# Kernel tuning notes

Hardware: AMD Instinct MI355X
Metric: run time of the kernel (lower is better)

The kernel has to match this reference:

```python
import jax, jax.numpy as jnp
import numpy as np

D_MODEL = 1024
HEAD_DIM = D_MODEL // 16  # num_heads=16, used only for the softmax scale
EPS = 1e-5


def _layernorm(x, g, b):
    mu = jnp.mean(x, axis=-1, keepdims=True)
    var = jnp.var(x, axis=-1, keepdims=True)
    return (x - mu) * jax.lax.rsqrt(var + EPS) * g + b


def setup_inputs() -> dict:
    key = jax.random.key(0)
    ks = jax.random.split(key, 16)
    d, dff = D_MODEL, 4 * D_MODEL
    s = 1.0 / np.sqrt(d)
    inp = {
        "x": jax.random.normal(ks[0], (4, 2048, d), dtype=jnp.float32),
        "wq": jax.random.normal(ks[1], (d, d), dtype=jnp.float32) * s,
        "bq": jnp.zeros((d,), jnp.float32),
        "wk": jax.random.normal(ks[2], (d, d), dtype=jnp.float32) * s,
        "bk": jnp.zeros((d,), jnp.float32),
        "wv": jax.random.normal(ks[3], (d, d), dtype=jnp.float32) * s,
        "bv": jnp.zeros((d,), jnp.float32),
        "wo": jax.random.normal(ks[4], (d, d), dtype=jnp.float32) * s,
        "bo": jnp.zeros((d,), jnp.float32),
        "w1": jax.random.normal(ks[5], (d, dff), dtype=jnp.float32) * s,
        "b1": jnp.zeros((dff,), jnp.float32),
        "w2": jax.random.normal(ks[6], (dff, d), dtype=jnp.float32) * (1.0 / np.sqrt(dff)),
        "b2": jnp.zeros((d,), jnp.float32),
        "g1": jnp.ones((d,), jnp.float32),
        "be1": jnp.zeros((d,), jnp.float32),
        "g2": jnp.ones((d,), jnp.float32),
        "be2": jnp.zeros((d,), jnp.float32),
    }
    return inp


def reference(x, wq, bq, wk, bk, wv, bv, wo, bo, w1, b1, w2, b2, g1, be1, g2, be2):
    # --- attention sub-block (NOTE: no head split in original module) ---
    residual = x
    h = _layernorm(x, g1, be1)
    q = h @ wq + bq
    k = h @ wk + bk
    v = h @ wv + bv
    scale = 1.0 / np.sqrt(HEAD_DIM)
    scores = jnp.einsum("bsd,btd->bst", q, k) * scale  # [B,S,S]
    attn = jax.nn.softmax(scores, axis=-1)
    ctx = jnp.einsum("bst,btd->bsd", attn, v)
    x = ctx @ wo + bo + residual
    # --- MLP sub-block ---
    residual = x
    h = _layernorm(x, g2, be2)
    h = jax.nn.gelu(h @ w1 + b1, approximate=False)
    return h @ w2 + b2 + residual
```

## Files before the change

### kernel.cpp

```cpp
#include <hip/hip_runtime.h>
#include <hip/hip_bf16.h>

typedef __hip_bfloat16 bf16;
typedef __attribute__((ext_vector_type(8))) short short8;
typedef __attribute__((ext_vector_type(4))) float floatx4;

__device__ __forceinline__ unsigned short f2bf(float x) {
  unsigned u = __builtin_bit_cast(unsigned, x);
  unsigned r = (u + 0x7fffu + ((u >> 16) & 1u)) >> 16;
  return (unsigned short)r;
}

#define GLL(g, l) __builtin_amdgcn_global_load_lds(                                  \
    (const __attribute__((address_space(1))) void*)(g),                              \
    (__attribute__((address_space(3))) void*)(l), 16, 0, 0)

__global__ __launch_bounds__(256) void wtrans_kernel(const float* __restrict__ in,
                                                     bf16* __restrict__ out,
                                                     int K, int N) {
  __shared__ float tile[32][33];
  int tx = threadIdx.x, ty = threadIdx.y;
  int n0 = blockIdx.x * 32, k0 = blockIdx.y * 32;
#pragma unroll
  for (int i = 0; i < 32; i += 8)
    tile[ty + i][tx] = in[(size_t)(k0 + ty + i) * N + (n0 + tx)];
  __syncthreads();
#pragma unroll
  for (int i = 0; i < 32; i += 8)
    out[(size_t)(n0 + ty + i) * K + (k0 + tx)] = __float2bfloat16(tile[tx][ty + i]);
}

__global__ __launch_bounds__(256) void btrans_kernel(const bf16* __restrict__ in,
                                                     int ldin, size_t sIn,
                                                     bf16* __restrict__ out,
                                                     int ldout, size_t sOut) {
  __shared__ bf16 tile[32][33];
  int tx = threadIdx.x, ty = threadIdx.y;
  int c0 = blockIdx.x * 32, r0 = blockIdx.y * 32;
  size_t bi = sIn * blockIdx.z, bo = sOut * blockIdx.z;
#pragma unroll
  for (int i = 0; i < 32; i += 8)
    tile[ty + i][tx] = in[bi + (size_t)(r0 + ty + i) * ldin + (c0 + tx)];
  __syncthreads();
#pragma unroll
  for (int i = 0; i < 32; i += 8)
    out[bo + (size_t)(c0 + ty + i) * ldout + (r0 + tx)] = tile[tx][ty + i];
}

__global__ __launch_bounds__(256) void ln_kernel(const float* __restrict__ x,
                                                 const float* __restrict__ g,
                                                 const float* __restrict__ b,
                                                 bf16* __restrict__ out) {
  const int D = 1024;
  size_t row = blockIdx.x;
  int t = threadIdx.x;
  float4 v = ((const float4*)(x + row * D))[t];
  float s  = v.x + v.y + v.z + v.w;
  float ss = v.x * v.x + v.y * v.y + v.z * v.z + v.w * v.w;
#pragma unroll
  for (int off = 32; off > 0; off >>= 1) {
    s  += __shfl_xor(s, off);
    ss += __shfl_xor(ss, off);
  }
  __shared__ float rs[4], rss[4];
  int wv = t >> 6;
  if ((t & 63) == 0) { rs[wv] = s; rss[wv] = ss; }
  __syncthreads();
  s  = rs[0] + rs[1] + rs[2] + rs[3];
  ss = rss[0] + rss[1] + rss[2] + rss[3];
  float mu  = s * (1.f / D);
  float inv = rsqrtf(ss * (1.f / D) - mu * mu + 1e-5f);
  float4 gv = ((const float4*)g)[t];
  float4 bv = ((const float4*)b)[t];
  ushort4 o;
  o.x = f2bf((v.x - mu) * inv * gv.x + bv.x);
  o.y = f2bf((v.y - mu) * inv * gv.y + bv.y);
  o.z = f2bf((v.z - mu) * inv * gv.z + bv.z);
  o.w = f2bf((v.w - mu) * inv * gv.w + bv.w);
  ((ushort4*)(out + row * D))[t] = o;
}

__global__ __launch_bounds__(256) void softmax_kernel(float* sc) {
  const int S = 2048;
  float* p = sc + (size_t)blockIdx.x * S;
  int t = threadIdx.x;
  float4 v0 = ((const float4*)p)[2 * t];
  float4 v1 = ((const float4*)p)[2 * t + 1];
  float f[8] = {v0.x, v0.y, v0.z, v0.w, v1.x, v1.y, v1.z, v1.w};
  float m = f[0];
#pragma unroll
  for (int j = 1; j < 8; ++j) m = fmaxf(m, f[j]);
#pragma unroll
  for (int off = 32; off > 0; off >>= 1) m = fmaxf(m, __shfl_xor(m, off));
  __shared__ float r1[4], r2[4];
  int wv = t >> 6;
  if ((t & 63) == 0) r1[wv] = m;
  __syncthreads();
  m = fmaxf(fmaxf(r1[0], r1[1]), fmaxf(r1[2], r1[3]));
  float s = 0.f;
#pragma unroll
  for (int j = 0; j < 8; ++j) { f[j] = __expf(f[j] - m); s += f[j]; }
#pragma unroll
  for (int off = 32; off > 0; off >>= 1) s += __shfl_xor(s, off);
  if ((t & 63) == 0) r2[wv] = s;
  __syncthreads();
  s = r2[0] + r2[1] + r2[2] + r2[3];
  float inv = 1.f / s;
  unsigned u0 = f2bf(f[0] * inv), u1 = f2bf(f[1] * inv);
  unsigned u2 = f2bf(f[2] * inv), u3 = f2bf(f[3] * inv);
  unsigned u4 = f2bf(f[4] * inv), u5 = f2bf(f[5] * inv);
  unsigned u6 = f2bf(f[6] * inv), u7 = f2bf(f[7] * inv);
  uint4 o;
  o.x = u0 | (u1 << 16);
  o.y = u2 | (u3 << 16);
  o.z = u4 | (u5 << 16);
  o.w = u6 | (u7 << 16);
  ((uint4*)p)[t] = o;
}

template <int NF, bool OUT_BF16, bool HAS_BIAS, bool HAS_RES, bool GELU>
__global__ __launch_bounds__(512, 2) void gemm8p(
    const bf16* __restrict__ A, int lda, size_t sA,
    const bf16* __restrict__ BT, int ldb, size_t sB,
    void* Cv, size_t sC,
    const float* __restrict__ bias, const float* res,
    int N, int K, float alpha, int gx, int gy) {
  constexpr int BN = NF * 64;
  constexpr int LB = NF / 2;
  constexpr int VM = 4 + 3 * LB;
  constexpr int BSLOT = BN * 64;
  __shared__ char lds[65536 + 4 * BSLOT + 1024];
  char* const ldsA = lds;
  char* const ldsB = lds + 65536;
  char* const ldsScr = lds + 65536 + 4 * BSLOT;

  const int tid = threadIdx.x;
  const int lane = tid & 63;
  const int wave = tid >> 6;
  const int wm = wave >> 2, wn = wave & 3;
  const int lr = lane & 15, lq = lane >> 4;

  int id = blockIdx.x;
  const int nwg = gridDim.x;
  if ((nwg & 7) == 0) id = (id & 7) * (nwg >> 3) + (id >> 3);
  const int bx = id % gx;
  const int rem = id / gx;
  const int by = rem % gy;
  const int bz = rem / gy;
  const int m0 = by * 256, n0 = bx * BN;

  const int wrow = wave * 16 + (lane >> 2);
  const int swzc = ((lane & 3) ^ ((lane >> 2) & 3)) * 8;
  const bf16* gA = A + sA * bz + (size_t)(m0 + wrow) * lda + swzc;
  const bf16* gB = BT + sB * bz + (size_t)(n0 + wrow) * ldb + swzc;

  const int nk = K >> 6;

  const int aBase = (wm * 128 + lr) * 64 + ((lq ^ (lr & 3)) << 4);
  const int bBase = (wn * (NF * 16) + lr) * 64 + ((lq ^ (lr & 3)) << 4);

  auto stA = [&](int tau, int h) {
    const int tc = tau < nk ? tau : nk - 1;
    const bf16* s = gA + (size_t)tc * 64 + h * 32;
    if (tau < nk) {
      char* d = ldsA + (((tau & 1) * 2 + h) << 14) + tid * 16;
      GLL(s, d);
      GLL(s + (size_t)128 * lda, d + 8192);
    } else {
      char* d = ldsScr + (lane << 4);
      GLL(s, d);
      GLL(s, d);
    }
  };
  auto stB = [&](int tau, int h) {
    const int tc = tau < nk ? tau : nk - 1;
    const bf16* s = gB + (size_t)tc * 64 + h * 32;
    if (tau < nk) {
      char* d = ldsB + ((tau & 1) * 2 + h) * BSLOT + tid * 16;
      GLL(s, d);
      if constexpr (NF == 4) GLL(s + (size_t)128 * ldb, d + 8192);
    } else {
      char* d = ldsScr + (lane << 4);
      GLL(s, d);
      if constexpr (NF == 4) GLL(s, d);
    }
  };

  floatx4 acc[8][NF] = {};

  stB(0, 0); stA(0, 0); stB(0, 1); stA(0, 1);
  stB(1, 0); stA(1, 0); stB(1, 1);
  asm volatile("s_waitcnt vmcnt(%0)" ::"i"(VM) : "memory");
  __builtin_amdgcn_s_barrier();

  for (int t = 0; t < nk; ++t) {
    const char* Ak0 = ldsA + (((t & 1) * 2 + 0) << 14);
    const char* Ak1 = ldsA + (((t & 1) * 2 + 1) << 14);
    const char* Bk0 = ldsB + ((t & 1) * 2 + 0) * BSLOT;
    const char* Bk1 = ldsB + ((t & 1) * 2 + 1) * BSLOT;

    short8 b0[NF], a0[4];
#pragma unroll
    for (int ni = 0; ni < NF; ++ni) b0[ni] = *(const short8*)(Bk0 + bBase + ni * 1024);
#pragma unroll
    for (int mi = 0; mi < 4; ++mi) a0[mi] = *(const short8*)(Ak0 + aBase + mi * 1024);
    stA(t + 1, 1);
    __builtin_amdgcn_s_barrier();
    asm volatile("s_waitcnt lgkmcnt(0)" ::: "memory");
    __builtin_amdgcn_sched_barrier(0);
    __builtin_amdgcn_s_setprio(1);
#pragma unroll
    for (int mi = 0; mi < 4; ++mi)
#pragma unroll
      for (int ni = 0; ni < NF; ++ni)
        acc[mi][ni] = __builtin_amdgcn_mfma_f32_16x16x32_bf16(a0[mi], b0[ni], acc[mi][ni], 0, 0, 0);
    __builtin_amdgcn_s_setprio(0);
    __builtin_amdgcn_s_barrier();

    short8 a1[4];
#pragma unroll
    for (int mi = 0; mi < 4; ++mi) a1[mi] = *(const short8*)(Ak0 + aBase + 4096 + mi * 1024);
    stB(t + 2, 0);
    __builtin_amdgcn_s_barrier();
    asm volatile("s_waitcnt lgkmcnt(0)" ::: "memory");
    __builtin_amdgcn_sched_barrier(0);
    __builtin_amdgcn_s_setprio(1);
#pragma unroll
    for (int mi = 0; mi < 4; ++mi)
#pragma unroll
      for (int ni = 0; ni < NF; ++ni)
        acc[4 + mi][ni] = __builtin_amdgcn_mfma_f32_16x16x32_bf16(a1[mi], b0[ni], acc[4 + mi][ni], 0, 0, 0);
    __builtin_amdgcn_s_setprio(0);
    asm volatile("s_waitcnt vmcnt(%0)" ::"i"(VM) : "memory");
    __builtin_amdgcn_s_barrier();

    short8 b1[NF], a2[4];
#pragma unroll
    for (int ni = 0; ni < NF; ++ni) b1[ni] = *(const short8*)(Bk1 + bBase + ni * 1024);
#pragma unroll
    for (int mi = 0; mi < 4; ++mi) a2[mi] = *(const short8*)(Ak1 + aBase + mi * 1024);
    stA(t + 2, 0);
    __builtin_amdgcn_s_barrier();
    asm volatile("s_waitcnt lgkmcnt(0)" ::: "memory");
    __builtin_amdgcn_sched_barrier(0);
    __builtin_amdgcn_s_setprio(1);
#pragma unroll
    for (int mi = 0; mi < 4; ++mi)
#pragma unroll
      for (int ni = 0; ni < NF; ++ni)
        acc[mi][ni] = __builtin_amdgcn_mfma_f32_16x16x32_bf16(a2[mi], b1[ni], acc[mi][ni], 0, 0, 0);
    __builtin_amdgcn_s_setprio(0);
    __builtin_amdgcn_s_barrier();

    short8 a3[4];
#pragma unroll
    for (int mi = 0; mi < 4; ++mi) a3[mi] = *(const short8*)(Ak1 + aBase + 4096 + mi * 1024);
    stB(t + 2, 1);
    __builtin_amdgcn_s_barrier();
    asm volatile("s_waitcnt lgkmcnt(0)" ::: "memory");
    __builtin_amdgcn_sched_barrier(0);
    __builtin_amdgcn_s_setprio(1);
#pragma unroll
    for (int mi = 0; mi < 4; ++mi)
#pragma unroll
      for (int ni = 0; ni < NF; ++ni)
        acc[4 + mi][ni] = __builtin_amdgcn_mfma_f32_16x16x32_bf16(a3[mi], b1[ni], acc[4 + mi][ni], 0, 0, 0);
    __builtin_amdgcn_s_setprio(0);
    asm volatile("s_waitcnt vmcnt(%0)" ::"i"(VM) : "memory");
    __builtin_amdgcn_s_barrier();
  }
  asm volatile("s_waitcnt vmcnt(0)" ::: "memory");

  float* Cf = (float*)Cv;
  bf16* Cb = (bf16*)Cv;
  const size_t cb = sC * bz;
#pragma unroll
  for (int mi = 0; mi < 8; ++mi) {
    const int row = m0 + wm * 128 + mi * 16 + lq * 4;
#pragma unroll
    for (int ni = 0; ni < NF; ++ni) {
      const int col = n0 + wn * (NF * 16) + ni * 16 + lr;
      const float bb = HAS_BIAS ? bias[col] : 0.f;
#pragma unroll
      for (int r = 0; r < 4; ++r) {
        float val = acc[mi][ni][r] * alpha + bb;
        if (GELU) val = 0.5f * val * (1.f + erff(val * 0.70710678118654752f));
        if (HAS_RES) val += res[(size_t)(row + r) * N + col];
        const size_t idx = cb + (size_t)(row + r) * N + col;
        if (OUT_BF16) Cb[idx] = __float2bfloat16(val);
        else Cf[idx] = val;
      }
    }
  }
}

extern "C" void kernel_launch(void* const* d_in, const int* in_sizes, int n_in,
                              void* d_out, int out_size, void* d_ws, size_t ws_size,
                              hipStream_t stream) {
  const int B = 4, S = 2048, D = 1024, DFF = 4096;
  const int M = B * S;
  const float* x   = (const float*)d_in[0];
  const float* wq  = (const float*)d_in[1];
  const float* bq  = (const float*)d_in[2];
  const float* wk  = (const float*)d_in[3];
  const float* bk  = (const float*)d_in[4];
  const float* wv  = (const float*)d_in[5];
  const float* bv  = (const float*)d_in[6];
  const float* wo  = (const float*)d_in[7];
  const float* bo  = (const float*)d_in[8];
  const float* w1  = (const float*)d_in[9];
  const float* b1  = (const float*)d_in[10];
  const float* w2  = (const float*)d_in[11];
  const float* b2  = (const float*)d_in[12];
  const float* g1  = (const float*)d_in[13];
  const float* be1 = (const float*)d_in[14];
  const float* g2  = (const float*)d_in[15];
  const float* be2 = (const float*)d_in[16];
  float* out = (float*)d_out;

  char* wsb = (char*)d_ws;
  const size_t MB1 = 1ull << 20;
  bf16* wqkvT = (bf16*)(wsb + 0 * MB1);
  bf16* woT   = (bf16*)(wsb + 6 * MB1);
  bf16* w1T   = (bf16*)(wsb + 8 * MB1);
  bf16* w2T   = (bf16*)(wsb + 16 * MB1);
  float* bqkv = (float*)(wsb + 24 * MB1);
  bf16* h     = (bf16*)(wsb + 25 * MB1);
  bf16* qkv   = (bf16*)(wsb + 41 * MB1);
  bf16* hidden = (bf16*)(wsb + 41 * MB1);
  char* attn  = wsb + 89 * MB1;

  int chunk = 1;
  if (ws_size > 89 * MB1) {
    size_t c = (ws_size - 89 * MB1) / (20 * MB1);
    chunk = (int)(c > 4 ? 4 : (c < 1 ? 1 : c));
  }
  bf16* vTc = (bf16*)attn;
  float* sc = (float*)(attn + (size_t)chunk * 4 * MB1);

  dim3 tb(32, 8);
  wtrans_kernel<<<dim3(32, 32), tb, 0, stream>>>(wq, wqkvT, D, D);
  wtrans_kernel<<<dim3(32, 32), tb, 0, stream>>>(wk, wqkvT + (size_t)1024 * 1024, D, D);
  wtrans_kernel<<<dim3(32, 32), tb, 0, stream>>>(wv, wqkvT + (size_t)2048 * 1024, D, D);
  wtrans_kernel<<<dim3(32, 32), tb, 0, stream>>>(wo, woT, D, D);
  wtrans_kernel<<<dim3(128, 32), tb, 0, stream>>>(w1, w1T, D, DFF);
  wtrans_kernel<<<dim3(32, 128), tb, 0, stream>>>(w2, w2T, DFF, D);
  hipMemcpyAsync(bqkv, bq, 4096, hipMemcpyDeviceToDevice, stream);
  hipMemcpyAsync(bqkv + 1024, bk, 4096, hipMemcpyDeviceToDevice, stream);
  hipMemcpyAsync(bqkv + 2048, bv, 4096, hipMemcpyDeviceToDevice, stream);

  ln_kernel<<<M, 256, 0, stream>>>(x, g1, be1, h);

  gemm8p<2, true, true, false, false><<<24 * 32, 512, 0, stream>>>(
      h, D, 0, wqkvT, D, 0, qkv, 0, bqkv, nullptr, 3072, D, 1.f, 24, 32);

  for (int b0 = 0; b0 < B; b0 += chunk) {
    int c = (B - b0 < chunk) ? (B - b0) : chunk;
    btrans_kernel<<<dim3(32, 64, c), tb, 0, stream>>>(
        qkv + (size_t)b0 * S * 3072 + 2048, 3072, (size_t)S * 3072,
        vTc, S, (size_t)D * S);
    gemm8p<4, false, false, false, false><<<64 * c, 512, 0, stream>>>(
        qkv + (size_t)b0 * S * 3072, 3072, (size_t)S * 3072,
        qkv + (size_t)b0 * S * 3072 + 1024, 3072, (size_t)S * 3072,
        sc, (size_t)S * S, nullptr, nullptr, S, D, 0.125f, 8, 8);
    softmax_kernel<<<c * S, 256, 0, stream>>>(sc);
    gemm8p<2, true, false, false, false><<<64 * c, 512, 0, stream>>>(
        (const bf16*)sc, 2 * S, (size_t)S * 2 * S,
        vTc, S, (size_t)D * S,
        h + (size_t)b0 * S * D, (size_t)S * D, nullptr, nullptr, D, S, 1.f, 8, 8);
  }

  gemm8p<2, false, true, true, false><<<8 * 32, 512, 0, stream>>>(
      h, D, 0, woT, D, 0, out, 0, bo, x, D, D, 1.f, 8, 32);

  ln_kernel<<<M, 256, 0, stream>>>(out, g2, be2, h);

  gemm8p<4, true, true, false, true><<<16 * 32, 512, 0, stream>>>(
      h, D, 0, w1T, D, 0, hidden, 0, b1, nullptr, DFF, D, 1.f, 16, 32);

  gemm8p<2, false, true, true, false><<<8 * 32, 512, 0, stream>>>(
      hidden, DFF, 0, w2T, DFF, 0, out, 0, b2, out, D, DFF, 1.f, 8, 32);
}
```

Before: 492.0 us.

## Restructure GEMM into quadrant-pipelined tiles and fuse V transpose into QKV epilogue

```diff
diff --git a/kernel.cpp b/kernel.cpp
--- a/kernel.cpp
+++ b/kernel.cpp
@@ -14,6 +14,10 @@
 #define GLL(g, l) __builtin_amdgcn_global_load_lds(                                  \
     (const __attribute__((address_space(1))) void*)(g),                              \
     (__attribute__((address_space(3))) void*)(l), 16, 0, 0)
+
+template <int N> __device__ __forceinline__ void vmwait() {
+  asm volatile("s_waitcnt vmcnt(%0)" ::"i"(N) : "memory");
+}
 
 __global__ __launch_bounds__(256) void wtrans_kernel(const float* __restrict__ in,
                                                      bf16* __restrict__ out,
@@ -28,23 +32,6 @@
 #pragma unroll
   for (int i = 0; i < 32; i += 8)
     out[(size_t)(n0 + ty + i) * K + (k0 + tx)] = __float2bfloat16(tile[tx][ty + i]);
-}
-
-__global__ __launch_bounds__(256) void btrans_kernel(const bf16* __restrict__ in,
-                                                     int ldin, size_t sIn,
-                                                     bf16* __restrict__ out,
-                                                     int ldout, size_t sOut) {
-  __shared__ bf16 tile[32][33];
-  int tx = threadIdx.x, ty = threadIdx.y;
-  int c0 = blockIdx.x * 32, r0 = blockIdx.y * 32;
-  size_t bi = sIn * blockIdx.z, bo = sOut * blockIdx.z;
-#pragma unroll
-  for (int i = 0; i < 32; i += 8)
-    tile[ty + i][tx] = in[bi + (size_t)(r0 + ty + i) * ldin + (c0 + tx)];
-  __syncthreads();
-#pragma unroll
-  for (int i = 0; i < 32; i += 8)
-    out[bo + (size_t)(c0 + ty + i) * ldout + (r0 + tx)] = tile[tx][ty + i];
 }
 
 __global__ __launch_bounds__(256) void ln_kernel(const float* __restrict__ x,
@@ -118,21 +105,21 @@
   ((uint4*)p)[t] = o;
 }
 
-template <int NF, bool OUT_BF16, bool HAS_BIAS, bool HAS_RES, bool GELU>
-__global__ __launch_bounds__(512, 2) void gemm8p(
+template <int NF, bool OUT_BF16, bool HAS_BIAS, bool HAS_RES, bool GELU, bool VTR>
+__global__ __launch_bounds__(512, 2) void gemm4q(
     const bf16* __restrict__ A, int lda, size_t sA,
     const bf16* __restrict__ BT, int ldb, size_t sB,
     void* Cv, size_t sC,
-    const float* __restrict__ bias, const float* res,
+    const float* __restrict__ bias, const float* res, bf16* vtr,
     int N, int K, float alpha, int gx, int gy) {
   constexpr int BN = NF * 64;
-  constexpr int LB = NF / 2;
-  constexpr int VM = 4 + 3 * LB;
-  constexpr int BSLOT = BN * 64;
-  __shared__ char lds[65536 + 4 * BSLOT + 1024];
+  constexpr int NI = NF / 2;
+  constexpr int BHALF = NF == 4 ? 16384 : 8192;
+  constexpr int W_A = 4;
+  constexpr int W_B = NF == 4 ? 4 : 3;
+  __shared__ __align__(16) char lds[65536 + (NF == 4 ? 65536 : 32768)];
   char* const ldsA = lds;
   char* const ldsB = lds + 65536;
-  char* const ldsScr = lds + 65536 + 4 * BSLOT;
 
   const int tid = threadIdx.x;
   const int lane = tid & 63;
@@ -149,149 +136,178 @@
   const int bz = rem / gy;
   const int m0 = by * 256, n0 = bx * BN;
 
-  const int wrow = wave * 16 + (lane >> 2);
-  const int swzc = ((lane & 3) ^ ((lane >> 2) & 3)) * 8;
-  const bf16* gA = A + sA * bz + (size_t)(m0 + wrow) * lda + swzc;
-  const bf16* gB = BT + sB * bz + (size_t)(n0 + wrow) * ldb + swzc;
+  const int srow = tid >> 3;
+  const int schunk = ((tid & 7) ^ (srow & 7)) * 8;
+  const bf16* gA = A + sA * bz + (size_t)(m0 + srow) * lda + schunk;
+  const bf16* gB = BT + sB * bz + (size_t)(n0 + srow) * ldb + schunk;
 
   const int nk = K >> 6;
 
-  const int aBase = (wm * 128 + lr) * 64 + ((lq ^ (lr & 3)) << 4);
-  const int bBase = (wn * (NF * 16) + lr) * 64 + ((lq ^ (lr & 3)) << 4);
-
-  auto stA = [&](int tau, int h) {
-    const int tc = tau < nk ? tau : nk - 1;
-    const bf16* s = gA + (size_t)tc * 64 + h * 32;
-    if (tau < nk) {
-      char* d = ldsA + (((tau & 1) * 2 + h) << 14) + tid * 16;
+  auto stA = [&](int tt, int h) {
+    if (tt < nk) {
+      const bf16* s = gA + (size_t)(h * 128) * lda + (size_t)tt * 64;
+      char* d = ldsA + (((tt & 1) * 2 + h) << 14) + tid * 16;
       GLL(s, d);
-      GLL(s + (size_t)128 * lda, d + 8192);
-    } else {
-      char* d = ldsScr + (lane << 4);
+      GLL(s + (size_t)64 * lda, d + 8192);
+    }
+  };
+  auto stB = [&](int tt, int h) {
+    if (tt < nk) {
+      const bf16* s = gB + (size_t)(h * (BN / 2)) * ldb + (size_t)tt * 64;
+      char* d = ldsB + ((tt & 1) * 2 + h) * BHALF + tid * 16;
       GLL(s, d);
-      GLL(s, d);
+      if constexpr (NF == 4) GLL(s + (size_t)64 * ldb, d + 8192);
     }
   };
-  auto stB = [&](int tau, int h) {
-    const int tc = tau < nk ? tau : nk - 1;
-    const bf16* s = gB + (size_t)tc * 64 + h * 32;
-    if (tau < nk) {
-      char* d = ldsB + ((tau & 1) * 2 + h) * BSLOT + tid * 16;
-      GLL(s, d);
-      if constexpr (NF == 4) GLL(s + (size_t)128 * ldb, d + 8192);
-    } else {
-      char* d = ldsScr + (lane << 4);
-      GLL(s, d);
-      if constexpr (NF == 4) GLL(s, d);
-    }
-  };
-
-  floatx4 acc[8][NF] = {};
-
-  stB(0, 0); stA(0, 0); stB(0, 1); stA(0, 1);
-  stB(1, 0); stA(1, 0); stB(1, 1);
-  asm volatile("s_waitcnt vmcnt(%0)" ::"i"(VM) : "memory");
+
+  const int aB0 = (wm * 64 + lr) * 128 + ((lq ^ (lr & 7)) << 4);
+  const int aB1 = aB0 ^ 64;
+  const int bRow = (NF == 4) ? (wn * 32 + lr) : (wn * 16 + lr);
+  const int bB0 = bRow * 128 + ((lq ^ (lr & 7)) << 4);
+  const int bB1 = bB0 ^ 64;
+
+  floatx4 acc[2][2][4][NI] = {};
+
+  stA(0, 0); stB(0, 0); stB(0, 1); stA(0, 1);
+  vmwait<W_B>();
   __builtin_amdgcn_s_barrier();
 
   for (int t = 0; t < nk; ++t) {
-    const char* Ak0 = ldsA + (((t & 1) * 2 + 0) << 14);
-    const char* Ak1 = ldsA + (((t & 1) * 2 + 1) << 14);
-    const char* Bk0 = ldsB + ((t & 1) * 2 + 0) * BSLOT;
-    const char* Bk1 = ldsB + ((t & 1) * 2 + 1) * BSLOT;
-
-    short8 b0[NF], a0[4];
-#pragma unroll
-    for (int ni = 0; ni < NF; ++ni) b0[ni] = *(const short8*)(Bk0 + bBase + ni * 1024);
-#pragma unroll
-    for (int mi = 0; mi < 4; ++mi) a0[mi] = *(const short8*)(Ak0 + aBase + mi * 1024);
-    stA(t + 1, 1);
-    __builtin_amdgcn_s_barrier();
+    const char* As0 = ldsA + (((t & 1) * 2 + 0) << 14);
+    const char* As1 = ldsA + (((t & 1) * 2 + 1) << 14);
+    const char* Bs0 = ldsB + ((t & 1) * 2 + 0) * BHALF;
+    const char* Bs1 = ldsB + ((t & 1) * 2 + 1) * BHALF;
+    short8 a0[4], a1[4], b0[NI], b1[NI];
+
+#pragma unroll
+    for (int mi = 0; mi < 4; ++mi) {
+      a0[mi] = *(const short8*)(As0 + aB0 + mi * 2048);
+      a1[mi] = *(const short8*)(As0 + aB1 + mi * 2048);
+    }
+#pragma unroll
+    for (int ni = 0; ni < NI; ++ni) {
+      b0[ni] = *(const short8*)(Bs0 + bB0 + ni * 2048);
+      b1[ni] = *(const short8*)(Bs0 + bB1 + ni * 2048);
+    }
+    stA(t + 1, 0);
     asm volatile("s_waitcnt lgkmcnt(0)" ::: "memory");
     __builtin_amdgcn_sched_barrier(0);
     __builtin_amdgcn_s_setprio(1);
 #pragma unroll
     for (int mi = 0; mi < 4; ++mi)
 #pragma unroll
-      for (int ni = 0; ni < NF; ++ni)
-        acc[mi][ni] = __builtin_amdgcn_mfma_f32_16x16x32_bf16(a0[mi], b0[ni], acc[mi][ni], 0, 0, 0);
+      for (int ni = 0; ni < NI; ++ni)
+        acc[0][0][mi][ni] = __builtin_amdgcn_mfma_f32_16x16x32_bf16(a0[mi], b0[ni], acc[0][0][mi][ni], 0, 0, 0);
+#pragma unroll
+    for (int mi = 0; mi < 4; ++mi)
+#pragma unroll
+      for (int ni = 0; ni < NI; ++ni)
+        acc[0][0][mi][ni] = __builtin_amdgcn_mfma_f32_16x16x32_bf16(a1[mi], b1[ni], acc[0][0][mi][ni], 0, 0, 0);
     __builtin_amdgcn_s_setprio(0);
+    vmwait<W_A>();
     __builtin_amdgcn_s_barrier();
 
-    short8 a1[4];
-#pragma unroll
-    for (int mi = 0; mi < 4; ++mi) a1[mi] = *(const short8*)(Ak0 + aBase + 4096 + mi * 1024);
-    stB(t + 2, 0);
-    __builtin_amdgcn_s_barrier();
+#pragma unroll
+    for (int ni = 0; ni < NI; ++ni) {
+      b0[ni] = *(const short8*)(Bs1 + bB0 + ni * 2048);
+      b1[ni] = *(const short8*)(Bs1 + bB1 + ni * 2048);
+    }
+    stB(t + 1, 0);
     asm volatile("s_waitcnt lgkmcnt(0)" ::: "memory");
     __builtin_amdgcn_sched_barrier(0);
     __builtin_amdgcn_s_setprio(1);
 #pragma unroll
     for (int mi = 0; mi < 4; ++mi)
 #pragma unroll
-      for (int ni = 0; ni < NF; ++ni)
-        acc[4 + mi][ni] = __builtin_amdgcn_mfma_f32_16x16x32_bf16(a1[mi], b0[ni], acc[4 + mi][ni], 0, 0, 0);
+      for (int ni = 0; ni < NI; ++ni)
+        acc[0][1][mi][ni] = __builtin_amdgcn_mfma_f32_16x16x32_bf16(a0[mi], b0[ni], acc[0][1][mi][ni], 0, 0, 0);
+#pragma unroll
+    for (int mi = 0; mi < 4; ++mi)
+#pragma unroll
+      for (int ni = 0; ni < NI; ++ni)
+        acc[0][1][mi][ni] = __builtin_amdgcn_mfma_f32_16x16x32_bf16(a1[mi], b1[ni], acc[0][1][mi][ni], 0, 0, 0);
     __builtin_amdgcn_s_setprio(0);
-    asm volatile("s_waitcnt vmcnt(%0)" ::"i"(VM) : "memory");
+    vmwait<W_B>();
     __builtin_amdgcn_s_barrier();
 
-    short8 b1[NF], a2[4];
-#pragma unroll
-    for (int ni = 0; ni < NF; ++ni) b1[ni] = *(const short8*)(Bk1 + bBase + ni * 1024);
-#pragma unroll
-    for (int mi = 0; mi < 4; ++mi) a2[mi] = *(const short8*)(Ak1 + aBase + mi * 1024);
-    stA(t + 2, 0);
-    __builtin_amdgcn_s_barrier();
+#pragma unroll
+    for (int mi = 0; mi < 4; ++mi) {
+      a0[mi] = *(const short8*)(As1 + aB0 + mi * 2048);
+      a1[mi] = *(const short8*)(As1 + aB1 + mi * 2048);
+    }
+    stB(t + 1, 1);
     asm volatile("s_waitcnt lgkmcnt(0)" ::: "memory");
     __builtin_amdgcn_sched_barrier(0);
     __builtin_amdgcn_s_setprio(1);
 #pragma unroll
     for (int mi = 0; mi < 4; ++mi)
 #pragma unroll
-      for (int ni = 0; ni < NF; ++ni)
-        acc[mi][ni] = __builtin_amdgcn_mfma_f32_16x16x32_bf16(a2[mi], b1[ni], acc[mi][ni], 0, 0, 0);
+      for (int ni = 0; ni < NI; ++ni)
+        acc[1][1][mi][ni] = __builtin_amdgcn_mfma_f32_16x16x32_bf16(a0[mi], b0[ni], acc[1][1][mi][ni], 0, 0, 0);
+#pragma unroll
+    for (int mi = 0; mi < 4; ++mi)
+#pragma unroll
+      for (int ni = 0; ni < NI; ++ni)
+        acc[1][1][mi][ni] = __builtin_amdgcn_mfma_f32_16x16x32_bf16(a1[mi], b1[ni], acc[1][1][mi][ni], 0, 0, 0);
     __builtin_amdgcn_s_setprio(0);
     __builtin_amdgcn_s_barrier();
 
-    short8 a3[4];
-#pragma unroll
-    for (int mi = 0; mi < 4; ++mi) a3[mi] = *(const short8*)(Ak1 + aBase + 4096 + mi * 1024);
-    stB(t + 2, 1);
-    __builtin_amdgcn_s_barrier();
+#pragma unroll
+    for (int ni = 0; ni < NI; ++ni) {
+      b0[ni] = *(const short8*)(Bs0 + bB0 + ni * 2048);
+      b1[ni] = *(const short8*)(Bs0 + bB1 + ni * 2048);
+    }
+    stA(t + 1, 1);
     asm volatile("s_waitcnt lgkmcnt(0)" ::: "memory");
     __builtin_amdgcn_sched_barrier(0);
     __builtin_amdgcn_s_setprio(1);
 #pragma unroll
     for (int mi = 0; mi < 4; ++mi)
 #pragma unroll
-      for (int ni = 0; ni < NF; ++ni)
-        acc[4 + mi][ni] = __builtin_amdgcn_mfma_f32_16x16x32_bf16(a3[mi], b1[ni], acc[4 + mi][ni], 0, 0, 0);
+      for (int ni = 0; ni < NI; ++ni)
+        acc[1][0][mi][ni] = __builtin_amdgcn_mfma_f32_16x16x32_bf16(a0[mi], b0[ni], acc[1][0][mi][ni], 0, 0, 0);
+#pragma unroll
+    for (int mi = 0; mi < 4; ++mi)
+#pragma unroll
+      for (int ni = 0; ni < NI; ++ni)
+        acc[1][0][mi][ni] = __builtin_amdgcn_mfma_f32_16x16x32_bf16(a1[mi], b1[ni], acc[1][0][mi][ni], 0, 0, 0);
     __builtin_amdgcn_s_setprio(0);
-    asm volatile("s_waitcnt vmcnt(%0)" ::"i"(VM) : "memory");
+    vmwait<W_B>();
     __builtin_amdgcn_s_barrier();
   }
-  asm volatile("s_waitcnt vmcnt(0)" ::: "memory");
 
   float* Cf = (float*)Cv;
   bf16* Cb = (bf16*)Cv;
   const size_t cb = sC * bz;
 #pragma unroll
-  for (int mi = 0; mi < 8; ++mi) {
-    const int row = m0 + wm * 128 + mi * 16 + lq * 4;
-#pragma unroll
-    for (int ni = 0; ni < NF; ++ni) {
-      const int col = n0 + wn * (NF * 16) + ni * 16 + lr;
-      const float bb = HAS_BIAS ? bias[col] : 0.f;
-#pragma unroll
-      for (int r = 0; r < 4; ++r) {
-        float val = acc[mi][ni][r] * alpha + bb;
-        if (GELU) val = 0.5f * val * (1.f + erff(val * 0.70710678118654752f));
-        if (HAS_RES) val += res[(size_t)(row + r) * N + col];
-        const size_t idx = cb + (size_t)(row + r) * N + col;
-        if (OUT_BF16) Cb[idx] = __float2bfloat16(val);
-        else Cf[idx] = val;
+  for (int mq = 0; mq < 2; ++mq)
+#pragma unroll
+    for (int nq = 0; nq < 2; ++nq)
+#pragma unroll
+      for (int mi = 0; mi < 4; ++mi) {
+        const int row = m0 + mq * 128 + wm * 64 + mi * 16 + lq * 4;
+#pragma unroll
+        for (int ni = 0; ni < NI; ++ni) {
+          const int col = n0 + nq * (BN / 2) + wn * (BN / 8) + ni * 16 + lr;
+          const float bb = HAS_BIAS ? bias[col] : 0.f;
+#pragma unroll
+          for (int r = 0; r < 4; ++r) {
+            float val = acc[mq][nq][mi][ni][r] * alpha + bb;
+            if (GELU) val = 0.5f * val * (1.f + erff(val * 0.70710678118654752f));
+            if (HAS_RES) val += res[(size_t)(row + r) * N + col];
+            const size_t idx = cb + (size_t)(row + r) * N + col;
+            if (OUT_BF16) Cb[idx] = __float2bfloat16(val);
+            else Cf[idx] = val;
+            if (VTR) {
+              if (col >= 2048) {
+                const int rr = row + r;
+                vtr[(((size_t)(rr >> 11) << 10) + (col - 2048)) * 2048 + (rr & 2047)] =
+                    __float2bfloat16(val);
+              }
+            }
+          }
+        }
       }
-    }
-  }
 }
 
 extern "C" void kernel_launch(void* const* d_in, const int* in_sizes, int n_in,
@@ -328,15 +344,14 @@
   bf16* h     = (bf16*)(wsb + 25 * MB1);
   bf16* qkv   = (bf16*)(wsb + 41 * MB1);
   bf16* hidden = (bf16*)(wsb + 41 * MB1);
-  char* attn  = wsb + 89 * MB1;
+  bf16* vTall = (bf16*)(wsb + 89 * MB1);
+  float* sc   = (float*)(wsb + 105 * MB1);
 
   int chunk = 1;
-  if (ws_size > 89 * MB1) {
-    size_t c = (ws_size - 89 * MB1) / (20 * MB1);
+  if (ws_size > 105 * MB1) {
+    size_t c = (ws_size - 105 * MB1) / (16 * MB1);
     chunk = (int)(c > 4 ? 4 : (c < 1 ? 1 : c));
   }
-  bf16* vTc = (bf16*)attn;
-  float* sc = (float*)(attn + (size_t)chunk * 4 * MB1);
 
   dim3 tb(32, 8);
   wtrans_kernel<<<dim3(32, 32), tb, 0, stream>>>(wq, wqkvT, D, D);
@@ -351,33 +366,30 @@
 
   ln_kernel<<<M, 256, 0, stream>>>(x, g1, be1, h);
 
-  gemm8p<2, true, true, false, false><<<24 * 32, 512, 0, stream>>>(
-      h, D, 0, wqkvT, D, 0, qkv, 0, bqkv, nullptr, 3072, D, 1.f, 24, 32);
+  gemm4q<2, true, true, false, false, true><<<24 * 32, 512, 0, stream>>>(
+      h, D, 0, wqkvT, D, 0, qkv, 0, bqkv, nullptr, vTall, 3072, D, 1.f, 24, 32);
 
   for (int b0 = 0; b0 < B; b0 += chunk) {
     int c = (B - b0 < chunk) ? (B - b0) : chunk;
-    btrans_kernel<<<dim3(32, 64, c), tb, 0, stream>>>(
-        qkv + (size_t)b0 * S * 3072 + 2048, 3072, (size_t)S * 3072,
-        vTc, S, (size_t)D * S);
-    gemm8p<4, false, false, false, false><<<64 * c, 512, 0, stream>>>(
+    gemm4q<4, false, false, false, false, false><<<64 * c, 512, 0, stream>>>(
         qkv + (size_t)b0 * S * 3072, 3072, (size_t)S * 3072,
         qkv + (size_t)b0 * S * 3072 + 1024, 3072, (size_t)S * 3072,
-        sc, (size_t)S * S, nullptr, nullptr, S, D, 0.125f, 8, 8);
+        sc, (size_t)S * S, nullptr, nullptr, nullptr, S, D, 0.125f, 8, 8);
     softmax_kernel<<<c * S, 256, 0, stream>>>(sc);
-    gemm8p<2, true, false, false, false><<<64 * c, 512, 0, stream>>>(
+    gemm4q<2, true, false, false, false, false><<<64 * c, 512, 0, stream>>>(
         (const bf16*)sc, 2 * S, (size_t)S * 2 * S,
-        vTc, S, (size_t)D * S,
-        h + (size_t)b0 * S * D, (size_t)S * D, nullptr, nullptr, D, S, 1.f, 8, 8);
+        vTall + (size_t)b0 * D * S, S, (size_t)D * S,
+        h + (size_t)b0 * S * D, (size_t)S * D, nullptr, nullptr, nullptr, D, S, 1.f, 8, 8);
   }
 
-  gemm8p<2, false, true, true, false><<<8 * 32, 512, 0, stream>>>(
-      h, D, 0, woT, D, 0, out, 0, bo, x, D, D, 1.f, 8, 32);
+  gemm4q<2, false, true, true, false, false><<<8 * 32, 512, 0, stream>>>(
+      h, D, 0, woT, D, 0, out, 0, bo, x, nullptr, D, D, 1.f, 8, 32);
 
   ln_kernel<<<M, 256, 0, stream>>>(out, g2, be2, h);
 
-  gemm8p<4, true, true, false, true><<<16 * 32, 512, 0, stream>>>(
-      h, D, 0, w1T, D, 0, hidden, 0, b1, nullptr, DFF, D, 1.f, 16, 32);
-
-  gemm8p<2, false, true, true, false><<<8 * 32, 512, 0, stream>>>(
-      hidden, DFF, 0, w2T, DFF, 0, out, 0, b2, out, D, DFF, 1.f, 8, 32);
-}
+  gemm4q<4, true, true, false, true, false><<<16 * 32, 512, 0, stream>>>(
+      h, D, 0, w1T, D, 0, hidden, 0, b1, nullptr, nullptr, DFF, D, 1.f, 16, 32);
+
+  gemm4q<2, false, true, true, false, false><<<8 * 32, 512, 0, stream>>>(
+      hidden, DFF, 0, w2T, DFF, 0, out, 0, b2, out, nullptr, D, DFF, 1.f, 8, 32);
+}
```

New measurement: 473.4 us. -3.8%, faster.
